# Performance work log

Hardware: AMD Instinct MI355X
Metric: run time of the kernel (lower is better)

## Reference

```python
import jax, jax.numpy as jnp
import numpy as np

EPS = 1e-8
NEG = -1e9


def setup_inputs() -> dict:
    key = jax.random.key(0)
    k = jax.random.split(key, 5)
    B, C, T, D = 32, 512, 2000, 128
    return {
        "x": jax.random.normal(k[0], (B, C, T), dtype=jnp.float32),
        "attn_w": jax.random.normal(k[1], (D, 3 * C), dtype=jnp.float32) * 0.02,
        "attn_b": jax.random.normal(k[2], (D,), dtype=jnp.float32) * 0.02,
        "ctx_w": jax.random.normal(k[3], (C, D), dtype=jnp.float32) * 0.02,
        "ctx_b": jax.random.normal(k[4], (C,), dtype=jnp.float32) * 0.02,
        "mask": jnp.ones((B, T), dtype=jnp.int32),
    }


def reference(x, attn_w, attn_b, ctx_w, ctx_b, mask):
    # x: (B, C, T); mask: (B, T) with 1 = valid frame
    m = mask.astype(x.dtype)[:, None, :]                      # (B, 1, T)
    lengths = jnp.sum(m, axis=2, keepdims=True)               # (B, 1, 1)
    mean = jnp.sum(x * m, axis=2, keepdims=True) / lengths    # (B, C, 1)
    var = jnp.sum(jnp.square(x - mean) * m, axis=2, keepdims=True) / lengths
    std = jnp.sqrt(jnp.clip(var, EPS))                        # (B, C, 1)
    # global context: concat [x, mean, std] along channels -> (B, 3C, T)
    T = x.shape[2]
    context = jnp.concatenate(
        [x, jnp.broadcast_to(mean, x.shape), jnp.broadcast_to(std, x.shape)], axis=1
    )
    # two 1x1 convs == channel GEMMs
    alpha = jnp.tanh(jnp.einsum("dc,bct->bdt", attn_w, context) + attn_b[None, :, None])
    alpha = jnp.einsum("cd,bdt->bct", ctx_w, alpha) + ctx_b[None, :, None]  # (B, C, T)
    alpha = jnp.where(m == 0, NEG, alpha)
    alpha = jax.nn.softmax(alpha, axis=2)
    pooled_mean = jnp.sum(alpha * x, axis=2)                  # (B, C)
    pooled_var = jnp.sum(alpha * jnp.square(x - pooled_mean[:, :, None]), axis=2)
    pooled_std = jnp.sqrt(jnp.clip(pooled_var, EPS))
    return jnp.concatenate([pooled_mean, pooled_std], axis=1)  # (B, 2C)
```

## Files before the change

### kernel.cpp

```cpp
#include <hip/hip_runtime.h>
#include <hip/hip_bf16.h>
#include <math.h>

#define EPSF 1e-8f
typedef __attribute__((ext_vector_type(8))) short short8;
typedef __attribute__((ext_vector_type(4))) float f32x4;

__device__ __forceinline__ float wred_sum(float v) {
#pragma unroll
  for (int o = 32; o > 0; o >>= 1) v += __shfl_down(v, o, 64);
  return v;
}

static __device__ __forceinline__ unsigned short f2bf(float f) {
  __hip_bfloat16 h = __float2bfloat16(f);
  return *reinterpret_cast<unsigned short*>(&h);
}
static __device__ __forceinline__ float bf2f(unsigned short u) {
  unsigned int v = ((unsigned int)u) << 16;
  float f;
  __builtin_memcpy(&f, &v, 4);
  return f;
}

__global__ __launch_bounds__(256) void k_zero(float* __restrict__ p, int n4) {
  int i = blockIdx.x * 256 + threadIdx.x;
  if (i < n4)
    *reinterpret_cast<float4*>(p + (size_t)i * 4) = (float4){0.f, 0.f, 0.f, 0.f};
}

__global__ __launch_bounds__(256) void k_convert(
    const float* __restrict__ attn_w, const float* __restrict__ ctx_w,
    unsigned short* __restrict__ awb, unsigned short* __restrict__ cwb, int C, int D) {
  int i = blockIdx.x * 256 + threadIdx.x;
  int DC = D * C;
  if (i < DC) {
    int d = i / C, c = i % C;
    awb[i] = f2bf(attn_w[(size_t)d * 3 * C + c]);
  } else if (i < 2 * DC) {
    int j = i - DC;
    cwb[j] = f2bf(ctx_w[j]);
  }
}

__global__ __launch_bounds__(256) void k_ms_tr(
    const float* __restrict__ x, const int* __restrict__ mask,
    float* __restrict__ sums, unsigned short* __restrict__ xbT, int C, int T) {
  int b = blockIdx.z, c0 = blockIdx.x * 64, t0 = blockIdx.y * 64;
  int tid = threadIdx.x;
  int row = tid >> 2, q = tid & 3;
  __shared__ float Xs[64][65];
  const float* xr = x + ((size_t)b * C + c0 + row) * T;
  const int* mr = mask + (size_t)b * T;
  float s1 = 0.f, s2 = 0.f;

#pragma unroll
  for (int ss = 0; ss < 4; ss++) {
    int cc = q + 4 * ss;
    int t = t0 + cc * 4;
    float4 v;
    float mv[4];
    if (t + 3 < T) {
      v = *reinterpret_cast<const float4*>(&xr[t]);
      int4 mm = *reinterpret_cast<const int4*>(&mr[t]);
      mv[0] = (float)mm.x; mv[1] = (float)mm.y; mv[2] = (float)mm.z; mv[3] = (float)mm.w;
    } else {
      v.x = (t < T) ? xr[t] : 0.f;     mv[0] = (t < T) ? (float)mr[t] : 0.f;
      v.y = (t+1 < T) ? xr[t+1] : 0.f; mv[1] = (t+1 < T) ? (float)mr[t+1] : 0.f;
      v.z = (t+2 < T) ? xr[t+2] : 0.f; mv[2] = (t+2 < T) ? (float)mr[t+2] : 0.f;
      v.w = (t+3 < T) ? xr[t+3] : 0.f; mv[3] = (t+3 < T) ? (float)mr[t+3] : 0.f;
    }
    s1 += mv[0]*v.x + mv[1]*v.y + mv[2]*v.z + mv[3]*v.w;
    s2 += mv[0]*v.x*v.x + mv[1]*v.y*v.y + mv[2]*v.z*v.z + mv[3]*v.w*v.w;
    int tl = cc * 4;
    Xs[row][tl+0] = v.x; Xs[row][tl+1] = v.y; Xs[row][tl+2] = v.z; Xs[row][tl+3] = v.w;
  }
  __syncthreads();
  {
    int trow = tid >> 2;
    int t = t0 + trow;
    if (t < T) {
      unsigned short buf[16];
#pragma unroll
      for (int m = 0; m < 16; m++) buf[m] = f2bf(Xs[q * 16 + m][trow]);
      unsigned short* dst = &xbT[((size_t)b * T + t) * C + c0 + q * 16];
      *reinterpret_cast<short8*>(dst) = *reinterpret_cast<short8*>(&buf[0]);
      *reinterpret_cast<short8*>(dst + 8) = *reinterpret_cast<short8*>(&buf[8]);
    }
  }
  s1 += __shfl_down(s1, 2, 4); s1 += __shfl_down(s1, 1, 4);
  s2 += __shfl_down(s2, 2, 4); s2 += __shfl_down(s2, 1, 4);
  if (q == 0) {
    float* sp = &sums[((size_t)b * C + c0 + row) * 2];
    atomicAdd(sp, s1);
    atomicAdd(sp + 1, s2);
  }
}

__global__ __launch_bounds__(256) void k_ms_fin(
    const float* __restrict__ sums, const int* __restrict__ mask,
    float* __restrict__ mean, float* __restrict__ stdv, int C, int T) {
  int b = blockIdx.x;
  int tid = threadIdx.x;
  const int* mr = mask + (size_t)b * T;
  float sl = 0.f;
  for (int t = tid; t < T; t += 256) sl += (float)mr[t];
  __shared__ float rl[4];
  sl = wred_sum(sl);
  if ((tid & 63) == 0) rl[tid >> 6] = sl;
  __syncthreads();
  float L = fmaxf(rl[0] + rl[1] + rl[2] + rl[3], 1.f);
  for (int c = tid; c < C; c += 256) {
    float s1 = sums[((size_t)b * C + c) * 2];
    float s2 = sums[((size_t)b * C + c) * 2 + 1];
    float mu = s1 / L;
    float var = s2 / L - mu * mu;
    mean[(size_t)b * C + c] = mu;
    stdv[(size_t)b * C + c] = sqrtf(fmaxf(var, EPSF));
  }
}

__global__ __launch_bounds__(256) void k_bias2(
    const float* __restrict__ attn_w, const float* __restrict__ attn_b,
    const float* __restrict__ mean, const float* __restrict__ stdv,
    float* __restrict__ bias2, int C, int D) {
  int bd = blockIdx.x;
  int b = bd / D;
  int d = bd % D;
  const float* wr = attn_w + (size_t)d * 3 * C;
  float s = 0.f;
  for (int c = threadIdx.x; c < C; c += 256)
    s += wr[C + c] * mean[(size_t)b * C + c] + wr[2 * C + c] * stdv[(size_t)b * C + c];
  __shared__ float r[4];
  s = wred_sum(s);
  if ((threadIdx.x & 63) == 0) r[threadIdx.x >> 6] = s;
  __syncthreads();
  if (threadIdx.x == 0) bias2[bd] = attn_b[d] + r[0] + r[1] + r[2] + r[3];
}

__global__ __launch_bounds__(256) void k_gemm1(
    const unsigned short* __restrict__ xbT, const unsigned short* __restrict__ awb,
    const float* __restrict__ bias2, unsigned short* __restrict__ alphaT,
    int C, int T, int D) {
  int b = blockIdx.y;
  int t0 = blockIdx.x * 128;
  int tid = threadIdx.x;
  int w = tid >> 6, lane = tid & 63;
  int wt0 = (w >> 1) * 64, wd0 = (w & 1) * 64;
  int l15 = lane & 15, g = lane >> 4;
  __shared__ unsigned short As[128][72];
  __shared__ unsigned short Bs[128][72];
  f32x4 acc[4][4];
#pragma unroll
  for (int i = 0; i < 4; i++)
#pragma unroll
    for (int j = 0; j < 4; j++) acc[i][j] = (f32x4){0.f, 0.f, 0.f, 0.f};

  int srow = tid >> 1, h = tid & 1;
  bool okA = (t0 + srow) < T;
  size_t rowA = ((size_t)b * T + t0 + srow) * C + h * 32;
  size_t rowB = (size_t)srow * C + h * 32;

  short8 ra[4], rb[4];
#pragma unroll
  for (int qq = 0; qq < 4; qq++) {
    ra[qq] = okA ? *reinterpret_cast<const short8*>(&xbT[rowA + qq * 8]) : (short8){};
    rb[qq] = *reinterpret_cast<const short8*>(&awb[rowB + qq * 8]);
  }

  for (int c0 = 0; c0 < C; c0 += 64) {
    __syncthreads();
#pragma unroll
    for (int qq = 0; qq < 4; qq++) {
      *reinterpret_cast<short8*>(&As[srow][h * 32 + qq * 8]) = ra[qq];
      *reinterpret_cast<short8*>(&Bs[srow][h * 32 + qq * 8]) = rb[qq];
    }
    if (c0 + 64 < C) {
      size_t nA = rowA + c0 + 64, nB = rowB + c0 + 64;
#pragma unroll
      for (int qq = 0; qq < 4; qq++) {
        ra[qq] = okA ? *reinterpret_cast<const short8*>(&xbT[nA + qq * 8]) : (short8){};
        rb[qq] = *reinterpret_cast<const short8*>(&awb[nB + qq * 8]);
      }
    }
    __syncthreads();
#pragma unroll
    for (int ks = 0; ks < 2; ks++) {
      short8 a[4], bb[4];
#pragma unroll
      for (int tf = 0; tf < 4; tf++)
        a[tf] = *reinterpret_cast<const short8*>(&As[wt0 + tf * 16 + l15][ks * 32 + g * 8]);
#pragma unroll
      for (int df = 0; df < 4; df++)
        bb[df] = *reinterpret_cast<const short8*>(&Bs[wd0 + df * 16 + l15][ks * 32 + g * 8]);
#pragma unroll
      for (int tf = 0; tf < 4; tf++)
#pragma unroll
        for (int df = 0; df < 4; df++)
          acc[tf][df] = __builtin_amdgcn_mfma_f32_16x16x32_bf16(a[tf], bb[df], acc[tf][df], 0, 0, 0);
    }
  }
#pragma unroll
  for (int df = 0; df < 4; df++) {
    int d = wd0 + df * 16 + l15;
    float bias = bias2[(size_t)b * D + d];
#pragma unroll
    for (int tf = 0; tf < 4; tf++)
#pragma unroll
      for (int r = 0; r < 4; r++) {
        int t = t0 + wt0 + tf * 16 + g * 4 + r;
        if (t < T)
          alphaT[((size_t)b * T + t) * D + d] = f2bf(tanhf(bias + acc[tf][df][r]));
      }
  }
}

__global__ __launch_bounds__(256) void k_pool2(
    const unsigned short* __restrict__ alphaT, const unsigned short* __restrict__ cwb,
    const unsigned short* __restrict__ xbT, const int* __restrict__ mask,
    float* __restrict__ Sacc, int C, int T, int D) {
  int b = blockIdx.z;
  int c0 = blockIdx.y * 64;
  int ch0 = blockIdx.x * 256;
  int tid = threadIdx.x;
  int w = tid >> 6, lane = tid & 63, l15 = lane & 15, g = lane >> 4;
  __shared__ unsigned short Bl[2][64][136];
  __shared__ unsigned short Xt[2][64][72];

  short8 a[4];
#pragma unroll
  for (int ks = 0; ks < 4; ks++)
    a[ks] = *reinterpret_cast<const short8*>(
        &cwb[(size_t)(c0 + w * 16 + l15) * D + ks * 32 + g * 8]);
  int cbase = c0 + w * 16 + g * 4;
  float S0[4] = {0.f, 0.f, 0.f, 0.f};
  float S1[4] = {0.f, 0.f, 0.f, 0.f};
  float S2[4] = {0.f, 0.f, 0.f, 0.f};

  const int* mr = mask + (size_t)b * T;
  int srow = tid >> 2, sq = tid & 3;

  int rem = T - ch0;
  int ntt = rem >= 256 ? 4 : (rem + 63) >> 6;

  short8 pa0, pa1, pa2, pa3, px0, px1;

#define LOADSUB(st)                                                            \
  {                                                                            \
    int trow = ch0 + (st) * 64 + srow;                                         \
    pa0 = pa1 = pa2 = pa3 = px0 = px1 = (short8){};                            \
    if (trow < T) {                                                            \
      const unsigned short* sa = &alphaT[((size_t)b * T + trow) * D + sq * 32];\
      pa0 = *reinterpret_cast<const short8*>(sa);                              \
      pa1 = *reinterpret_cast<const short8*>(sa + 8);                          \
      pa2 = *reinterpret_cast<const short8*>(sa + 16);                         \
      pa3 = *reinterpret_cast<const short8*>(sa + 24);                         \
      const unsigned short* sx = &xbT[((size_t)b * T + trow) * C + c0 + sq*16];\
      px0 = *reinterpret_cast<const short8*>(sx);                              \
      px1 = *reinterpret_cast<const short8*>(sx + 8);                          \
    }                                                                          \
  }

#define WRITESUB(bufi)                                                         \
  {                                                                            \
    *reinterpret_cast<short8*>(&Bl[bufi][srow][sq * 32]) = pa0;                \
    *reinterpret_cast<short8*>(&Bl[bufi][srow][sq * 32 + 8]) = pa1;            \
    *reinterpret_cast<short8*>(&Bl[bufi][srow][sq * 32 + 16]) = pa2;           \
    *reinterpret_cast<short8*>(&Bl[bufi][srow][sq * 32 + 24]) = pa3;           \
    *reinterpret_cast<short8*>(&Xt[bufi][srow][sq * 16]) = px0;                \
    *reinterpret_cast<short8*>(&Xt[bufi][srow][sq * 16 + 8]) = px1;            \
  }

  LOADSUB(0);
  WRITESUB(0);
  if (ntt > 1) LOADSUB(1);
  __syncthreads();

  for (int k = 0; k < ntt; k++) {
    int buf = k & 1;
    if (k + 1 < ntt) {
      WRITESUB((k + 1) & 1);
      if (k + 2 < ntt) LOADSUB(k + 2);
    }
    int t0 = ch0 + k * 64;
#pragma unroll
    for (int tf = 0; tf < 4; tf++) {
      f32x4 p = (f32x4){0.f, 0.f, 0.f, 0.f};
#pragma unroll
      for (int ks = 0; ks < 4; ks++) {
        short8 bb = *reinterpret_cast<const short8*>(
            &Bl[buf][tf * 16 + l15][ks * 32 + g * 8]);
        p = __builtin_amdgcn_mfma_f32_16x16x32_bf16(a[ks], bb, p, 0, 0, 0);
      }
      int t = t0 + tf * 16 + l15;
      bool valid = (t < T) && (mr[t < T ? t : 0] != 0);
#pragma unroll
      for (int r = 0; r < 4; r++) {
        float e = valid ? __expf(p[r]) : 0.f;
        float xv = bf2f(Xt[buf][tf * 16 + l15][w * 16 + g * 4 + r]);
        S0[r] += e; S1[r] += e * xv; S2[r] += e * xv * xv;
      }
    }
    __syncthreads();
  }
#undef LOADSUB
#undef WRITESUB

#pragma unroll
  for (int r = 0; r < 4; r++) {
#pragma unroll
    for (int o = 1; o < 16; o <<= 1) {
      S0[r] += __shfl_xor(S0[r], o, 16);
      S1[r] += __shfl_xor(S1[r], o, 16);
      S2[r] += __shfl_xor(S2[r], o, 16);
    }
  }
  if (l15 == 0) {
#pragma unroll
    for (int r = 0; r < 4; r++) {
      float* sp = &Sacc[((size_t)b * C + cbase + r) * 3];
      atomicAdd(sp, S0[r]);
      atomicAdd(sp + 1, S1[r]);
      atomicAdd(sp + 2, S2[r]);
    }
  }
}

__global__ __launch_bounds__(256) void k_out(
    const float* __restrict__ Sacc, float* __restrict__ out, int C) {
  int b = blockIdx.x;
  for (int c = threadIdx.x; c < C; c += 256) {
    float S0 = Sacc[((size_t)b * C + c) * 3];
    float S1 = Sacc[((size_t)b * C + c) * 3 + 1];
    float S2 = Sacc[((size_t)b * C + c) * 3 + 2];
    float pm = S1 / S0;
    float var = S2 / S0 - pm * pm;
    out[(size_t)b * 2 * C + c] = pm;
    out[(size_t)b * 2 * C + C + c] = sqrtf(fmaxf(var, EPSF));
  }
}

extern "C" void kernel_launch(void* const* d_in, const int* in_sizes, int n_in,
                              void* d_out, int out_size, void* d_ws, size_t ws_size,
                              hipStream_t stream) {
  const float* x = (const float*)d_in[0];
  const float* attn_w = (const float*)d_in[1];
  const float* attn_b = (const float*)d_in[2];
  const float* ctx_w = (const float*)d_in[3];
  const int* mask = (const int*)d_in[5];
  float* out = (float*)d_out;

  int D = in_sizes[2];
  int C = in_sizes[4];
  int B = out_size / (2 * C);
  int T = in_sizes[5] / B;

  unsigned short* awb = (unsigned short*)d_ws;
  unsigned short* cwb = awb + (size_t)D * C;
  float* mean = (float*)(cwb + (size_t)C * D);
  float* stdv = mean + (size_t)B * C;
  float* bias2 = stdv + (size_t)B * C;
  float* sums = bias2 + (size_t)B * D;
  float* Sacc = sums + (size_t)B * C * 2;
  unsigned short* xbT = (unsigned short*)(Sacc + (size_t)B * C * 3);
  unsigned short* alphaT = xbT + (size_t)B * T * C;

  int nzero4 = (B * C * 5 + 3) / 4;
  k_zero<<<(nzero4 + 255) / 256, 256, 0, stream>>>(sums, nzero4);
  k_convert<<<(2 * D * C + 255) / 256, 256, 0, stream>>>(attn_w, ctx_w, awb, cwb, C, D);
  k_ms_tr<<<dim3(C / 64, (T + 63) / 64, B), 256, 0, stream>>>(x, mask, sums, xbT, C, T);
  k_ms_fin<<<B, 256, 0, stream>>>(sums, mask, mean, stdv, C, T);
  k_bias2<<<B * D, 256, 0, stream>>>(attn_w, attn_b, mean, stdv, bias2, C, D);
  k_gemm1<<<dim3((T + 127) / 128, B), 256, 0, stream>>>(xbT, awb, bias2, alphaT, C, T, D);
  k_pool2<<<dim3((T + 255) / 256, C / 64, B), 256, 0, stream>>>(
      alphaT, cwb, xbT, mask, Sacc, C, T, D);
  k_out<<<B, 256, 0, stream>>>(Sacc, out, C);
}
```

Baseline: 142.9 us.

## Drop transposed bf16 copy of x; read fp32 x directly in GEMM and pooling

Removes the bf16 transposed xbT buffer written by the mean/std kernel. The attention GEMM and pooling kernels now read fp32 x directly, convert it to bf16 on the fly and transpose it through shared memory. The GEMM tile shrinks to 64 time steps with all 128 D columns per block. This removes one full write and reread of an intermediate tensor the size of x. In exchange x is read as fp32, twice the bytes of bf16, in both the GEMM and pooling passes, and the GEMM gains an extra shared-memory transpose step and barrier.

```diff
diff --git a/kernel.cpp b/kernel.cpp
--- a/kernel.cpp
+++ b/kernel.cpp
@@ -21,6 +21,28 @@
   float f;
   __builtin_memcpy(&f, &v, 4);
   return f;
+}
+
+__device__ __forceinline__ void load_x16(const float* __restrict__ xr, int ts, int T,
+                                         short8& lo, short8& hi) {
+  unsigned short xb[16];
+#pragma unroll
+  for (int m = 0; m < 4; m++) {
+    int t = ts + m * 4;
+    float4 v;
+    if (t + 3 < T) {
+      v = *reinterpret_cast<const float4*>(&xr[t]);
+    } else {
+      v.x = (t < T) ? xr[t] : 0.f;
+      v.y = (t + 1 < T) ? xr[t + 1] : 0.f;
+      v.z = (t + 2 < T) ? xr[t + 2] : 0.f;
+      v.w = (t + 3 < T) ? xr[t + 3] : 0.f;
+    }
+    xb[m * 4 + 0] = f2bf(v.x); xb[m * 4 + 1] = f2bf(v.y);
+    xb[m * 4 + 2] = f2bf(v.z); xb[m * 4 + 3] = f2bf(v.w);
+  }
+  lo = *reinterpret_cast<short8*>(&xb[0]);
+  hi = *reinterpret_cast<short8*>(&xb[8]);
 }
 
 __global__ __launch_bounds__(256) void k_zero(float* __restrict__ p, int n4) {
@@ -43,21 +65,18 @@
   }
 }
 
-__global__ __launch_bounds__(256) void k_ms_tr(
+__global__ __launch_bounds__(256) void k_ms(
     const float* __restrict__ x, const int* __restrict__ mask,
-    float* __restrict__ sums, unsigned short* __restrict__ xbT, int C, int T) {
+    float* __restrict__ sums, int C, int T) {
   int b = blockIdx.z, c0 = blockIdx.x * 64, t0 = blockIdx.y * 64;
   int tid = threadIdx.x;
   int row = tid >> 2, q = tid & 3;
-  __shared__ float Xs[64][65];
   const float* xr = x + ((size_t)b * C + c0 + row) * T;
   const int* mr = mask + (size_t)b * T;
   float s1 = 0.f, s2 = 0.f;
-
-#pragma unroll
-  for (int ss = 0; ss < 4; ss++) {
-    int cc = q + 4 * ss;
-    int t = t0 + cc * 4;
+#pragma unroll
+  for (int m = 0; m < 4; m++) {
+    int t = t0 + q * 16 + m * 4;
     float4 v;
     float mv[4];
     if (t + 3 < T) {
@@ -72,21 +91,6 @@
     }
     s1 += mv[0]*v.x + mv[1]*v.y + mv[2]*v.z + mv[3]*v.w;
     s2 += mv[0]*v.x*v.x + mv[1]*v.y*v.y + mv[2]*v.z*v.z + mv[3]*v.w*v.w;
-    int tl = cc * 4;
-    Xs[row][tl+0] = v.x; Xs[row][tl+1] = v.y; Xs[row][tl+2] = v.z; Xs[row][tl+3] = v.w;
-  }
-  __syncthreads();
-  {
-    int trow = tid >> 2;
-    int t = t0 + trow;
-    if (t < T) {
-      unsigned short buf[16];
-#pragma unroll
-      for (int m = 0; m < 16; m++) buf[m] = f2bf(Xs[q * 16 + m][trow]);
-      unsigned short* dst = &xbT[((size_t)b * T + t) * C + c0 + q * 16];
-      *reinterpret_cast<short8*>(dst) = *reinterpret_cast<short8*>(&buf[0]);
-      *reinterpret_cast<short8*>(dst + 8) = *reinterpret_cast<short8*>(&buf[8]);
-    }
   }
   s1 += __shfl_down(s1, 2, 4); s1 += __shfl_down(s1, 1, 4);
   s2 += __shfl_down(s2, 2, 4); s2 += __shfl_down(s2, 1, 4);
@@ -138,77 +142,82 @@
   if (threadIdx.x == 0) bias2[bd] = attn_b[d] + r[0] + r[1] + r[2] + r[3];
 }
 
-__global__ __launch_bounds__(256) void k_gemm1(
-    const unsigned short* __restrict__ xbT, const unsigned short* __restrict__ awb,
+__global__ __launch_bounds__(256) void k_gemm1x(
+    const float* __restrict__ x, const unsigned short* __restrict__ awb,
     const float* __restrict__ bias2, unsigned short* __restrict__ alphaT,
     int C, int T, int D) {
   int b = blockIdx.y;
-  int t0 = blockIdx.x * 128;
+  int t0 = blockIdx.x * 64;
   int tid = threadIdx.x;
   int w = tid >> 6, lane = tid & 63;
-  int wt0 = (w >> 1) * 64, wd0 = (w & 1) * 64;
   int l15 = lane & 15, g = lane >> 4;
-  __shared__ unsigned short As[128][72];
+  __shared__ unsigned short Xf[64][72];
+  __shared__ unsigned short As[64][72];
   __shared__ unsigned short Bs[128][72];
-  f32x4 acc[4][4];
+
+  f32x4 acc[4][2];
 #pragma unroll
   for (int i = 0; i < 4; i++)
 #pragma unroll
-    for (int j = 0; j < 4; j++) acc[i][j] = (f32x4){0.f, 0.f, 0.f, 0.f};
-
-  int srow = tid >> 1, h = tid & 1;
-  bool okA = (t0 + srow) < T;
-  size_t rowA = ((size_t)b * T + t0 + srow) * C + h * 32;
-  size_t rowB = (size_t)srow * C + h * 32;
-
-  short8 ra[4], rb[4];
-#pragma unroll
-  for (int qq = 0; qq < 4; qq++) {
-    ra[qq] = okA ? *reinterpret_cast<const short8*>(&xbT[rowA + qq * 8]) : (short8){};
-    rb[qq] = *reinterpret_cast<const short8*>(&awb[rowB + qq * 8]);
-  }
+    for (int j = 0; j < 2; j++) acc[i][j] = (f32x4){0.f, 0.f, 0.f, 0.f};
+
+  int cr = tid >> 2, q = tid & 3;
+  int dr = tid >> 1, h = tid & 1;
+
+  short8 rx0, rx1, rb[4];
+  load_x16(x + ((size_t)b * C + cr) * T, t0 + q * 16, T, rx0, rx1);
+#pragma unroll
+  for (int qq = 0; qq < 4; qq++)
+    rb[qq] = *reinterpret_cast<const short8*>(&awb[(size_t)dr * C + h * 32 + qq * 8]);
 
   for (int c0 = 0; c0 < C; c0 += 64) {
     __syncthreads();
-#pragma unroll
-    for (int qq = 0; qq < 4; qq++) {
-      *reinterpret_cast<short8*>(&As[srow][h * 32 + qq * 8]) = ra[qq];
-      *reinterpret_cast<short8*>(&Bs[srow][h * 32 + qq * 8]) = rb[qq];
-    }
+    *reinterpret_cast<short8*>(&Xf[cr][q * 16]) = rx0;
+    *reinterpret_cast<short8*>(&Xf[cr][q * 16 + 8]) = rx1;
+#pragma unroll
+    for (int qq = 0; qq < 4; qq++)
+      *reinterpret_cast<short8*>(&Bs[dr][h * 32 + qq * 8]) = rb[qq];
     if (c0 + 64 < C) {
-      size_t nA = rowA + c0 + 64, nB = rowB + c0 + 64;
-#pragma unroll
-      for (int qq = 0; qq < 4; qq++) {
-        ra[qq] = okA ? *reinterpret_cast<const short8*>(&xbT[nA + qq * 8]) : (short8){};
+      load_x16(x + ((size_t)b * C + c0 + 64 + cr) * T, t0 + q * 16, T, rx0, rx1);
+      size_t nB = (size_t)dr * C + c0 + 64 + h * 32;
+#pragma unroll
+      for (int qq = 0; qq < 4; qq++)
         rb[qq] = *reinterpret_cast<const short8*>(&awb[nB + qq * 8]);
-      }
     }
     __syncthreads();
+    {
+      unsigned short buf[16];
+#pragma unroll
+      for (int m = 0; m < 16; m++) buf[m] = Xf[q * 16 + m][cr];
+      *reinterpret_cast<short8*>(&As[cr][q * 16]) = *reinterpret_cast<short8*>(&buf[0]);
+      *reinterpret_cast<short8*>(&As[cr][q * 16 + 8]) = *reinterpret_cast<short8*>(&buf[8]);
+    }
+    __syncthreads();
 #pragma unroll
     for (int ks = 0; ks < 2; ks++) {
-      short8 a[4], bb[4];
+      short8 a[4], bb[2];
 #pragma unroll
       for (int tf = 0; tf < 4; tf++)
-        a[tf] = *reinterpret_cast<const short8*>(&As[wt0 + tf * 16 + l15][ks * 32 + g * 8]);
-#pragma unroll
-      for (int df = 0; df < 4; df++)
-        bb[df] = *reinterpret_cast<const short8*>(&Bs[wd0 + df * 16 + l15][ks * 32 + g * 8]);
+        a[tf] = *reinterpret_cast<const short8*>(&As[tf * 16 + l15][ks * 32 + g * 8]);
+#pragma unroll
+      for (int df = 0; df < 2; df++)
+        bb[df] = *reinterpret_cast<const short8*>(&Bs[w * 32 + df * 16 + l15][ks * 32 + g * 8]);
 #pragma unroll
       for (int tf = 0; tf < 4; tf++)
 #pragma unroll
-        for (int df = 0; df < 4; df++)
+        for (int df = 0; df < 2; df++)
           acc[tf][df] = __builtin_amdgcn_mfma_f32_16x16x32_bf16(a[tf], bb[df], acc[tf][df], 0, 0, 0);
     }
   }
 #pragma unroll
-  for (int df = 0; df < 4; df++) {
-    int d = wd0 + df * 16 + l15;
+  for (int df = 0; df < 2; df++) {
+    int d = w * 32 + df * 16 + l15;
     float bias = bias2[(size_t)b * D + d];
 #pragma unroll
     for (int tf = 0; tf < 4; tf++)
 #pragma unroll
       for (int r = 0; r < 4; r++) {
-        int t = t0 + wt0 + tf * 16 + g * 4 + r;
+        int t = t0 + tf * 16 + g * 4 + r;
         if (t < T)
           alphaT[((size_t)b * T + t) * D + d] = f2bf(tanhf(bias + acc[tf][df][r]));
       }
@@ -217,7 +226,7 @@
 
 __global__ __launch_bounds__(256) void k_pool2(
     const unsigned short* __restrict__ alphaT, const unsigned short* __restrict__ cwb,
-    const unsigned short* __restrict__ xbT, const int* __restrict__ mask,
+    const float* __restrict__ x, const int* __restrict__ mask,
     float* __restrict__ Sacc, int C, int T, int D) {
   int b = blockIdx.z;
   int c0 = blockIdx.y * 64;
@@ -225,7 +234,7 @@
   int tid = threadIdx.x;
   int w = tid >> 6, lane = tid & 63, l15 = lane & 15, g = lane >> 4;
   __shared__ unsigned short Bl[2][64][136];
-  __shared__ unsigned short Xt[2][64][72];
+  __shared__ unsigned short Xf[2][64][72];
 
   short8 a[4];
 #pragma unroll
@@ -239,6 +248,7 @@
 
   const int* mr = mask + (size_t)b * T;
   int srow = tid >> 2, sq = tid & 3;
+  const float* xrc = x + ((size_t)b * C + c0 + srow) * T;
 
   int rem = T - ch0;
   int ntt = rem >= 256 ? 4 : (rem + 63) >> 6;
@@ -248,17 +258,15 @@
 #define LOADSUB(st)                                                            \
   {                                                                            \
     int trow = ch0 + (st) * 64 + srow;                                         \
-    pa0 = pa1 = pa2 = pa3 = px0 = px1 = (short8){};                            \
+    pa0 = pa1 = pa2 = pa3 = (short8){};                                        \
     if (trow < T) {                                                            \
       const unsigned short* sa = &alphaT[((size_t)b * T + trow) * D + sq * 32];\
       pa0 = *reinterpret_cast<const short8*>(sa);                              \
       pa1 = *reinterpret_cast<const short8*>(sa + 8);                          \
       pa2 = *reinterpret_cast<const short8*>(sa + 16);                         \
       pa3 = *reinterpret_cast<const short8*>(sa + 24);                         \
-      const unsigned short* sx = &xbT[((size_t)b * T + trow) * C + c0 + sq*16];\
-      px0 = *reinterpret_cast<const short8*>(sx);                              \
-      px1 = *reinterpret_cast<const short8*>(sx + 8);                          \
     }                                                                          \
+    load_x16(xrc, ch0 + (st) * 64 + sq * 16, T, px0, px1);                     \
   }
 
 #define WRITESUB(bufi)                                                         \
@@ -267,8 +275,8 @@
     *reinterpret_cast<short8*>(&Bl[bufi][srow][sq * 32 + 8]) = pa1;            \
     *reinterpret_cast<short8*>(&Bl[bufi][srow][sq * 32 + 16]) = pa2;           \
     *reinterpret_cast<short8*>(&Bl[bufi][srow][sq * 32 + 24]) = pa3;           \
-    *reinterpret_cast<short8*>(&Xt[bufi][srow][sq * 16]) = px0;                \
-    *reinterpret_cast<short8*>(&Xt[bufi][srow][sq * 16 + 8]) = px1;            \
+    *reinterpret_cast<short8*>(&Xf[bufi][srow][sq * 16]) = px0;                \
+    *reinterpret_cast<short8*>(&Xf[bufi][srow][sq * 16 + 8]) = px1;            \
   }
 
   LOADSUB(0);
@@ -297,7 +305,7 @@
 #pragma unroll
       for (int r = 0; r < 4; r++) {
         float e = valid ? __expf(p[r]) : 0.f;
-        float xv = bf2f(Xt[buf][tf * 16 + l15][w * 16 + g * 4 + r]);
+        float xv = bf2f(Xf[buf][w * 16 + g * 4 + r][tf * 16 + l15]);
         S0[r] += e; S1[r] += e * xv; S2[r] += e * xv * xv;
       }
     }
@@ -362,17 +370,16 @@
   float* bias2 = stdv + (size_t)B * C;
   float* sums = bias2 + (size_t)B * D;
   float* Sacc = sums + (size_t)B * C * 2;
-  unsigned short* xbT = (unsigned short*)(Sacc + (size_t)B * C * 3);
-  unsigned short* alphaT = xbT + (size_t)B * T * C;
+  unsigned short* alphaT = (unsigned short*)(Sacc + (size_t)B * C * 3);
 
   int nzero4 = (B * C * 5 + 3) / 4;
   k_zero<<<(nzero4 + 255) / 256, 256, 0, stream>>>(sums, nzero4);
   k_convert<<<(2 * D * C + 255) / 256, 256, 0, stream>>>(attn_w, ctx_w, awb, cwb, C, D);
-  k_ms_tr<<<dim3(C / 64, (T + 63) / 64, B), 256, 0, stream>>>(x, mask, sums, xbT, C, T);
+  k_ms<<<dim3(C / 64, (T + 63) / 64, B), 256, 0, stream>>>(x, mask, sums, C, T);
   k_ms_fin<<<B, 256, 0, stream>>>(sums, mask, mean, stdv, C, T);
   k_bias2<<<B * D, 256, 0, stream>>>(attn_w, attn_b, mean, stdv, bias2, C, D);
-  k_gemm1<<<dim3((T + 127) / 128, B), 256, 0, stream>>>(xbT, awb, bias2, alphaT, C, T, D);
+  k_gemm1x<<<dim3((T + 63) / 64, B), 256, 0, stream>>>(x, awb, bias2, alphaT, C, T, D);
   k_pool2<<<dim3((T + 255) / 256, C / 64, B), 256, 0, stream>>>(
-      alphaT, cwb, xbT, mask, Sacc, C, T, D);
+      alphaT, cwb, x, mask, Sacc, C, T, D);
   k_out<<<B, 256, 0, stream>>>(Sacc, out, C);
 }
```

After: 168.3 us. 17.8% more time.
